# Kernel optimization log

Hardware: AMD Instinct MI355X
Metric: run time of the kernel (lower is better)

The kernel has to match this reference:

```python
import jax, jax.numpy as jnp
import numpy as np

INPUT_DIM = 64
HIDDEN_DIM = 32


def setup_inputs() -> dict:
    key = jax.random.key(0)
    ks = jax.random.split(key, 9)
    B, C, H, W = 8, INPUT_DIM, 64, 64
    s_in = 1.0 / np.sqrt(C)
    inp = {
        "h": jax.random.normal(ks[0], (B, C, H, W), dtype=jnp.float32),
        # 1x1 conv weights stored as [out, in]
        "wq": jax.random.uniform(ks[1], (HIDDEN_DIM, C), jnp.float32, -s_in, s_in),
        "bq": jax.random.uniform(ks[2], (HIDDEN_DIM,), jnp.float32, -s_in, s_in),
        "wk": jax.random.uniform(ks[3], (HIDDEN_DIM, C), jnp.float32, -s_in, s_in),
        "bk": jax.random.uniform(ks[4], (HIDDEN_DIM,), jnp.float32, -s_in, s_in),
        "wv": jax.random.uniform(ks[5], (C, C), jnp.float32, -s_in, s_in),
        "bv": jax.random.uniform(ks[6], (C,), jnp.float32, -s_in, s_in),
        "wz": jax.random.uniform(ks[7], (C, C), jnp.float32, -s_in, s_in),
        "bz": jax.random.uniform(ks[8], (C,), jnp.float32, -s_in, s_in),
    }
    return inp


def reference(h, wq, bq, wk, bk, wv, bv, wz, bz):
    B, C, H, W = h.shape
    N = H * W
    x = h.reshape(B, C, N)  # [B, C, N]
    # 1x1 convs == channel-wise linear maps
    q = jnp.einsum('oc,bcn->bno', wq, x) + bq          # [B, N, Dh]
    k = jnp.einsum('oc,bcn->bon', wk, x) + bk[:, None]  # [B, Dh, N]
    v = jnp.einsum('oc,bcn->bon', wv, x) + bv[:, None]  # [B, C, N]
    attn = jax.nn.softmax(jnp.einsum('bnd,bdm->bnm', q, k), axis=-1)  # [B, N, N]
    z = jnp.einsum('bnm,bcm->bcn', attn, v)             # [B, C, N]
    out = jnp.einsum('oc,bcn->bon', wz, z) + bz[:, None]
    return out.reshape(B, C, H, W) + h
```

## Files before the change

kernel.cpp:

```cpp
#include <hip/hip_runtime.h>
#include <stdint.h>

#define BATCH 8
#define CIN   64
#define DH    32
#define NTOK  4096
#define LOG2E 1.4426950408889634f

typedef float    f4   __attribute__((ext_vector_type(4)));
typedef short    s8v  __attribute__((ext_vector_type(8)));
typedef uint32_t u32;
typedef uint32_t u32x2 __attribute__((ext_vector_type(2)));
typedef uint32_t u32x4 __attribute__((ext_vector_type(4)));

static __device__ __forceinline__ short f2bf(float f) {
    union { float f; u32 u; } c; c.f = f;
    u32 u = c.u;
    u32 r = (u + 0x7fffu + ((u >> 16) & 1u)) >> 16;
    return (short)(r & 0xffffu);
}
static __device__ __forceinline__ u32 pk2(float a, float b) {
    return (u32)(uint16_t)f2bf(a) | ((u32)(uint16_t)f2bf(b) << 16);
}
static __device__ __forceinline__ u32 pktr(float a, float b) {
    union { float f; u32 u; } ca, cb; ca.f = a; cb.f = b;
#if __has_builtin(__builtin_amdgcn_perm)
    return __builtin_amdgcn_perm(cb.u, ca.u, 0x07060302u);
#else
    return (cb.u & 0xffff0000u) | (ca.u >> 16);
#endif
}
static __device__ __forceinline__ float bfhi(u32 u) {
    union { u32 u; float f; } c; c.u = u & 0xffff0000u; return c.f;
}
static __device__ __forceinline__ float bflo(u32 u) {
    union { u32 u; float f; } c; c.u = u << 16; return c.f;
}

__global__ __launch_bounds__(256) void proj_kernel(
    const float* __restrict__ h,
    const float* __restrict__ wq, const float* __restrict__ bq,
    const float* __restrict__ wk, const float* __restrict__ bk,
    const float* __restrict__ wv, const float* __restrict__ bv,
    short* __restrict__ qbf, short* __restrict__ kbf, short* __restrict__ vp)
{
    __shared__ short xT [64 * 72];
    __shared__ short wqs[32 * 72];
    __shared__ short wks[32 * 72];
    __shared__ short wvs[64 * 72];
    __shared__ short vls2[64 * 68];
    __shared__ float bqs[32], bks[32], bvs[64];

    const int t   = threadIdx.x;
    const int b   = blockIdx.x;
    const int nt0 = blockIdx.y * 64;

    {
        const int c  = t >> 2;
        const int ng = (t & 3) * 16;
        const float* src = h + ((size_t)(b * CIN + c)) * NTOK + nt0 + ng;
        f4 x0 = *(const f4*)(src + 0);
        f4 x1 = *(const f4*)(src + 4);
        f4 x2 = *(const f4*)(src + 8);
        f4 x3 = *(const f4*)(src + 12);
        #pragma unroll
        for (int i = 0; i < 4; ++i) {
            xT[(ng + 0  + i) * 72 + c] = f2bf(x0[i]);
            xT[(ng + 4  + i) * 72 + c] = f2bf(x1[i]);
            xT[(ng + 8  + i) * 72 + c] = f2bf(x2[i]);
            xT[(ng + 12 + i) * 72 + c] = f2bf(x3[i]);
        }
    }
    for (int idx = t; idx < 2048; idx += 256) {
        int o = idx >> 6, c = idx & 63;
        wqs[o * 72 + c] = f2bf(wq[idx] * LOG2E);
        wks[o * 72 + c] = f2bf(wk[idx]);
    }
    for (int idx = t; idx < 4096; idx += 256)
        wvs[(idx >> 6) * 72 + (idx & 63)] = f2bf(wv[idx]);
    if (t < 32) { bqs[t] = bq[t] * LOG2E; bks[t] = bk[t]; }
    if (t < 64) bvs[t] = bv[t];
    __syncthreads();

    const int w    = t >> 6;
    const int ln   = t & 15;
    const int quad = (t >> 4) & 3;
    const int nl   = w * 16 + ln;
    const int n    = nt0 + nl;
    const f4 zf4 = {0.f, 0.f, 0.f, 0.f};

    const s8v xb0 = *(const s8v*)&xT[nl * 72 + quad * 8];
    const s8v xb1 = *(const s8v*)&xT[nl * 72 + 32 + quad * 8];

    #pragma unroll
    for (int ot = 0; ot < 2; ++ot) {
        s8v a0 = *(const s8v*)&wqs[(ot * 16 + ln) * 72 + quad * 8];
        s8v a1 = *(const s8v*)&wqs[(ot * 16 + ln) * 72 + 32 + quad * 8];
        f4 d = __builtin_amdgcn_mfma_f32_16x16x32_bf16(a0, xb0, zf4, 0, 0, 0);
        d     = __builtin_amdgcn_mfma_f32_16x16x32_bf16(a1, xb1, d,  0, 0, 0);
        f4 bb = *(const f4*)&bqs[ot * 16 + quad * 4];
        u32x2 pw; pw[0] = pk2(d[0] + bb[0], d[1] + bb[1]);
                  pw[1] = pk2(d[2] + bb[2], d[3] + bb[3]);
        *(u32x2*)(qbf + ((size_t)(b * NTOK + n)) * DH + ot * 16 + quad * 4) = pw;

        s8v c0 = *(const s8v*)&wks[(ot * 16 + ln) * 72 + quad * 8];
        s8v c1 = *(const s8v*)&wks[(ot * 16 + ln) * 72 + 32 + quad * 8];
        f4 e = __builtin_amdgcn_mfma_f32_16x16x32_bf16(c0, xb0, zf4, 0, 0, 0);
        e     = __builtin_amdgcn_mfma_f32_16x16x32_bf16(c1, xb1, e,  0, 0, 0);
        f4 kb = *(const f4*)&bks[ot * 16 + quad * 4];
        u32x2 kw; kw[0] = pk2(e[0] + kb[0], e[1] + kb[1]);
                  kw[1] = pk2(e[2] + kb[2], e[3] + kb[3]);
        *(u32x2*)(kbf + ((size_t)(b * NTOK + n)) * DH + ot * 16 + quad * 4) = kw;
    }

    {
        const int p    = nl & 31;
        const int row  = (nl >> 5) * 32 + ((p >> 2) & 3) * 8
                       + (p >> 4) * 4 + (p & 3);
        short* vrow = &vls2[row * 68];
        #pragma unroll
        for (int ot = 0; ot < 4; ++ot) {
            s8v a0 = *(const s8v*)&wvs[(ot * 16 + ln) * 72 + quad * 8];
            s8v a1 = *(const s8v*)&wvs[(ot * 16 + ln) * 72 + 32 + quad * 8];
            f4 d = __builtin_amdgcn_mfma_f32_16x16x32_bf16(a0, xb0, zf4, 0, 0, 0);
            d     = __builtin_amdgcn_mfma_f32_16x16x32_bf16(a1, xb1, d,  0, 0, 0);
            const int ch = ot * 16 + quad * 4;
            u32x2 pw;
            pw[0] = pk2(d[0] + bvs[ch],     d[1] + bvs[ch + 1]);
            pw[1] = pk2(d[2] + bvs[ch + 2], d[3] + bvs[ch + 3]);
            *(u32x2*)&vrow[ch] = pw;
        }
    }
    __syncthreads();

    {
        const int g = t >> 5;
        const int r = t & 31;
        short tmp[16];
        #pragma unroll
        for (int j = 0; j < 8; ++j)
            #pragma unroll
            for (int cc = 0; cc < 2; ++cc)
                tmp[cc * 8 + j] = vls2[(g * 8 + j) * 68 + r * 2 + cc];
        u32x4* dst = (u32x4*)(vp + ((size_t)(b * 128 + blockIdx.y * 2) * 4) * 64 * 8);
        #pragma unroll
        for (int i = 0; i < 2; ++i)
            dst[t * 2 + i] = ((const u32x4*)tmp)[i];
    }
}

__global__ __launch_bounds__(256, 2) void attn_kernel(
    const float* __restrict__ h,  const float* __restrict__ wz,
    const float* __restrict__ bz,
    const short* __restrict__ qbf, const short* __restrict__ kbf,
    const short* __restrict__ vp,  float* __restrict__ out)
{
    __shared__ short accb[4][64][72];
    __shared__ short zbuf[64][72];
    __shared__ float lbuf[4][64];

    const int b    = blockIdx.x;
    const int qb0  = blockIdx.y * 64;
    const int tid  = threadIdx.x;
    const int w    = tid >> 6;
    const int lane = tid & 63;
    const int ln   = lane & 15;
    const int quad = lane >> 4;
    const f4 zf4 = {0.f, 0.f, 0.f, 0.f};

    s8v qf[4];
    #pragma unroll
    for (int f = 0; f < 4; ++f)
        qf[f] = *(const s8v*)(qbf + ((size_t)(b * NTOK + qb0 + f * 16 + ln)) * DH + quad * 8);

    f4 acc[4][4];
    f4 accl[4];
    #pragma unroll
    for (int f = 0; f < 4; ++f) {
        accl[f] = zf4;
        #pragma unroll
        for (int ct = 0; ct < 4; ++ct) acc[f][ct] = zf4;
    }
    s8v ones;
    #pragma unroll
    for (int j = 0; j < 8; ++j) ones[j] = (short)0x3F80;

    const short* kb2 = kbf + ((size_t)b * NTOK + w * 1024) * DH;
    const s8v*   vb2 = (const s8v*)(vp + (size_t)b * NTOK * CIN)
                     + (size_t)(w * 32) * 4 * 64;

    for (int kt = 0; kt < 1024; kt += 32) {
        const short* kp = kb2 + kt * DH;
        s8v kk0 = *(const s8v*)(kp + ln * DH + quad * 8);
        s8v kk1 = *(const s8v*)(kp + (16 + ln) * DH + quad * 8);
        const s8v* vg = vb2 + (size_t)((kt >> 5) * 4 + quad) * 64 + ln;
        s8v v0 = vg[0], v1 = vg[16], v2 = vg[32], v3 = vg[48];

        #pragma unroll
        for (int f = 0; f < 4; ++f) {
            f4 sa = __builtin_amdgcn_mfma_f32_16x16x32_bf16(kk0, qf[f], zf4, 0, 0, 0);
            f4 sb = __builtin_amdgcn_mfma_f32_16x16x32_bf16(kk1, qf[f], zf4, 0, 0, 0);
            f4 ea, eb;
            #pragma unroll
            for (int r = 0; r < 4; ++r) {
                ea[r] = __builtin_amdgcn_exp2f(sa[r]);
                eb[r] = __builtin_amdgcn_exp2f(sb[r]);
            }
            u32x4 pd;
            pd[0] = pktr(ea[0], ea[1]); pd[1] = pktr(ea[2], ea[3]);
            pd[2] = pktr(eb[0], eb[1]); pd[3] = pktr(eb[2], eb[3]);
            s8v pf = __builtin_bit_cast(s8v, pd);

            accl[f]   = __builtin_amdgcn_mfma_f32_16x16x32_bf16(ones, pf, accl[f],   0, 0, 0);
            acc[f][0] = __builtin_amdgcn_mfma_f32_16x16x32_bf16(v0,   pf, acc[f][0], 0, 0, 0);
            acc[f][1] = __builtin_amdgcn_mfma_f32_16x16x32_bf16(v1,   pf, acc[f][1], 0, 0, 0);
            acc[f][2] = __builtin_amdgcn_mfma_f32_16x16x32_bf16(v2,   pf, acc[f][2], 0, 0, 0);
            acc[f][3] = __builtin_amdgcn_mfma_f32_16x16x32_bf16(v3,   pf, acc[f][3], 0, 0, 0);
        }
    }

    if (quad == 0) {
        #pragma unroll
        for (int f = 0; f < 4; ++f) lbuf[w][f * 16 + ln] = accl[f][0];
    }
    #pragma unroll
    for (int f = 0; f < 4; ++f) {
        #pragma unroll
        for (int ct = 0; ct < 4; ++ct) {
            u32x2 pw;
            pw[0] = pk2(acc[f][ct][0], acc[f][ct][1]);
            pw[1] = pk2(acc[f][ct][2], acc[f][ct][3]);
            *(u32x2*)&accb[w][f * 16 + ln][ct * 16 + quad * 4] = pw;
        }
    }
    __syncthreads();

    {
        const int q   = tid >> 2;
        const int chg = (tid & 3) * 16;
        float ls = lbuf[0][q] + lbuf[1][q] + lbuf[2][q] + lbuf[3][q];
        float rl = __builtin_amdgcn_rcpf(ls);
        float zv[16];
        #pragma unroll
        for (int i = 0; i < 16; ++i) zv[i] = 0.f;
        #pragma unroll
        for (int w2 = 0; w2 < 4; ++w2) {
            u32x4 ua = *(u32x4*)&accb[w2][q][chg];
            u32x4 ub = *(u32x4*)&accb[w2][q][chg + 8];
            #pragma unroll
            for (int d = 0; d < 4; ++d) {
                zv[d * 2]     += bflo(ua[d]); zv[d * 2 + 1]     += bfhi(ua[d]);
                zv[8 + d * 2] += bflo(ub[d]); zv[8 + d * 2 + 1] += bfhi(ub[d]);
            }
        }
        u32x4 za, zb2;
        #pragma unroll
        for (int d = 0; d < 4; ++d) {
            za[d]  = pk2(zv[d * 2] * rl,     zv[d * 2 + 1] * rl);
            zb2[d] = pk2(zv[8 + d * 2] * rl, zv[8 + d * 2 + 1] * rl);
        }
        *(u32x4*)&zbuf[q][chg]     = za;
        *(u32x4*)&zbuf[q][chg + 8] = zb2;
    }
    __syncthreads();

    {
        const int ot = w;
        s8v wzf[2];
        #pragma unroll
        for (int half = 0; half < 2; ++half) {
            const float* wp = wz + (ot * 16 + ln) * 64 + half * 32 + quad * 8;
            f4 wa = *(const f4*)wp;
            f4 wb = *(const f4*)(wp + 4);
            u32x4 tt;
            tt[0] = pk2(wa[0], wa[1]); tt[1] = pk2(wa[2], wa[3]);
            tt[2] = pk2(wb[0], wb[1]); tt[3] = pk2(wb[2], wb[3]);
            wzf[half] = __builtin_bit_cast(s8v, tt);
        }
        f4 bzv = *(const f4*)(bz + ot * 16 + quad * 4);
        #pragma unroll
        for (int fi = 0; fi < 4; ++fi) {
            const int row = fi * 16 + ln;
            s8v z0 = *(const s8v*)&zbuf[row][quad * 8];
            s8v z1 = *(const s8v*)&zbuf[row][32 + quad * 8];
            f4 oa = __builtin_amdgcn_mfma_f32_16x16x32_bf16(wzf[0], z0, zf4, 0, 0, 0);
            oa     = __builtin_amdgcn_mfma_f32_16x16x32_bf16(wzf[1], z1, oa,  0, 0, 0);
            #pragma unroll
            for (int r = 0; r < 4; ++r) {
                size_t idx = ((size_t)(b * CIN + ot * 16 + quad * 4 + r)) * NTOK
                           + qb0 + row;
                out[idx] = oa[r] + bzv[r] + h[idx];
            }
        }
    }
}

extern "C" void kernel_launch(void* const* d_in, const int* in_sizes, int n_in,
                              void* d_out, int out_size, void* d_ws, size_t ws_size,
                              hipStream_t stream) {
    (void)in_sizes; (void)n_in; (void)out_size; (void)ws_size;
    const float* h  = (const float*)d_in[0];
    const float* wq = (const float*)d_in[1];
    const float* bq = (const float*)d_in[2];
    const float* wk = (const float*)d_in[3];
    const float* bk = (const float*)d_in[4];
    const float* wv = (const float*)d_in[5];
    const float* bv = (const float*)d_in[6];
    const float* wz = (const float*)d_in[7];
    const float* bz = (const float*)d_in[8];
    float* out = (float*)d_out;

    short* qbf = (short*)d_ws;
    short* kbf = qbf + (size_t)BATCH * NTOK * DH;
    short* vpw = kbf + (size_t)BATCH * NTOK * DH;

    proj_kernel<<<dim3(8, 64), dim3(256), 0, stream>>>(
        h, wq, bq, wk, bk, wv, bv, qbf, kbf, vpw);
    attn_kernel<<<dim3(8, 64), dim3(256), 0, stream>>>(
        h, wz, bz, qbf, kbf, vpw, out);
}
```

Measured before the change: 115.7 us.

## Share K/V tiles across two query groups via LDS staging in larger blocks

```diff
diff --git a/kernel.cpp b/kernel.cpp
--- a/kernel.cpp
+++ b/kernel.cpp
@@ -149,29 +149,37 @@
     }
 }
 
-__global__ __launch_bounds__(256, 2) void attn_kernel(
+__global__ __launch_bounds__(512, 2) void attn_kernel(
     const float* __restrict__ h,  const float* __restrict__ wz,
     const float* __restrict__ bz,
     const short* __restrict__ qbf, const short* __restrict__ kbf,
     const short* __restrict__ vp,  float* __restrict__ out)
 {
-    __shared__ short accb[4][64][72];
-    __shared__ short zbuf[64][72];
-    __shared__ float lbuf[4][64];
+    __shared__ short kst[4 * 3072];
+    __shared__ short accb[128 * 72];
+    __shared__ short zbuf[128 * 72];
+    __shared__ float lbuf[128];
 
     const int b    = blockIdx.x;
-    const int qb0  = blockIdx.y * 64;
+    const int qb0  = blockIdx.y * 128;
     const int tid  = threadIdx.x;
     const int w    = tid >> 6;
     const int lane = tid & 63;
     const int ln   = lane & 15;
     const int quad = lane >> 4;
+    const int qg   = w & 1;
+    const int kh   = w >> 1;
     const f4 zf4 = {0.f, 0.f, 0.f, 0.f};
 
+    short* stage = &kst[kh * 3072];
+    const short* kb = kbf + ((size_t)b * NTOK + kh * 1024) * DH;
+    const short* vb = vp  + (size_t)(b * 128 + kh * 32) * 4 * 64 * 8;
+
     s8v qf[4];
     #pragma unroll
     for (int f = 0; f < 4; ++f)
-        qf[f] = *(const s8v*)(qbf + ((size_t)(b * NTOK + qb0 + f * 16 + ln)) * DH + quad * 8);
+        qf[f] = *(const s8v*)(qbf +
+            ((size_t)(b * NTOK + qb0 + qg * 64 + f * 16 + ln)) * DH + quad * 8);
 
     f4 acc[4][4];
     f4 accl[4];
@@ -185,16 +193,41 @@
     #pragma unroll
     for (int j = 0; j < 8; ++j) ones[j] = (short)0x3F80;
 
-    const short* kb2 = kbf + ((size_t)b * NTOK + w * 1024) * DH;
-    const s8v*   vb2 = (const s8v*)(vp + (size_t)b * NTOK * CIN)
-                     + (size_t)(w * 32) * 4 * 64;
-
-    for (int kt = 0; kt < 1024; kt += 32) {
-        const short* kp = kb2 + kt * DH;
-        s8v kk0 = *(const s8v*)(kp + ln * DH + quad * 8);
-        s8v kk1 = *(const s8v*)(kp + (16 + ln) * DH + quad * 8);
-        const s8v* vg = vb2 + (size_t)((kt >> 5) * 4 + quad) * 64 + ln;
-        s8v v0 = vg[0], v1 = vg[16], v2 = vg[32], v3 = vg[48];
+    u32x4 r[3];
+    #pragma unroll
+    for (int j = 0; j < 3; ++j) {
+        const int c = qg * 3 + j;
+        const short* src = (c < 2) ? (kb + c * 512 + lane * 8)
+                                   : (vb + (c - 2) * 512 + lane * 8);
+        r[j] = *(const u32x4*)src;
+    }
+
+    for (int it = 0; it < 32; ++it) {
+        __syncthreads();
+        #pragma unroll
+        for (int j = 0; j < 3; ++j) {
+            const int c = qg * 3 + j;
+            *(u32x4*)&stage[c * 512 + lane * 8] = r[j];
+        }
+        __syncthreads();
+        if (it + 1 < 32) {
+            const short* ks = kb + (it + 1) * 1024;
+            const short* vs = vb + (it + 1) * 2048;
+            #pragma unroll
+            for (int j = 0; j < 3; ++j) {
+                const int c = qg * 3 + j;
+                const short* src = (c < 2) ? (ks + c * 512 + lane * 8)
+                                           : (vs + (c - 2) * 512 + lane * 8);
+                r[j] = *(const u32x4*)src;
+            }
+        }
+
+        s8v kk0 = *(const s8v*)&stage[ln * 32 + quad * 8];
+        s8v kk1 = *(const s8v*)&stage[(16 + ln) * 32 + quad * 8];
+        s8v v0 = *(const s8v*)&stage[1024 + (quad * 64 +  0 + ln) * 8];
+        s8v v1 = *(const s8v*)&stage[1024 + (quad * 64 + 16 + ln) * 8];
+        s8v v2 = *(const s8v*)&stage[1024 + (quad * 64 + 32 + ln) * 8];
+        s8v v3 = *(const s8v*)&stage[1024 + (quad * 64 + 48 + ln) * 8];
 
         #pragma unroll
         for (int f = 0; f < 4; ++f) {
@@ -202,9 +235,9 @@
             f4 sb = __builtin_amdgcn_mfma_f32_16x16x32_bf16(kk1, qf[f], zf4, 0, 0, 0);
             f4 ea, eb;
             #pragma unroll
-            for (int r = 0; r < 4; ++r) {
-                ea[r] = __builtin_amdgcn_exp2f(sa[r]);
-                eb[r] = __builtin_amdgcn_exp2f(sb[r]);
+            for (int rr = 0; rr < 4; ++rr) {
+                ea[rr] = __builtin_amdgcn_exp2f(sa[rr]);
+                eb[rr] = __builtin_amdgcn_exp2f(sb[rr]);
             }
             u32x4 pd;
             pd[0] = pktr(ea[0], ea[1]); pd[1] = pktr(ea[2], ea[3]);
@@ -219,53 +252,56 @@
         }
     }
 
-    if (quad == 0) {
-        #pragma unroll
-        for (int f = 0; f < 4; ++f) lbuf[w][f * 16 + ln] = accl[f][0];
-    }
-    #pragma unroll
-    for (int f = 0; f < 4; ++f) {
-        #pragma unroll
-        for (int ct = 0; ct < 4; ++ct) {
-            u32x2 pw;
-            pw[0] = pk2(acc[f][ct][0], acc[f][ct][1]);
-            pw[1] = pk2(acc[f][ct][2], acc[f][ct][3]);
-            *(u32x2*)&accb[w][f * 16 + ln][ct * 16 + quad * 4] = pw;
+    for (int ph = 1; ph < 4; ++ph) {
+        if (kh == ph) {
+            #pragma unroll
+            for (int f = 0; f < 4; ++f) {
+                const int row = qg * 64 + f * 16 + ln;
+                if (quad == 0) lbuf[row] = accl[f][0];
+                #pragma unroll
+                for (int ct = 0; ct < 4; ++ct) {
+                    u32x2 pw;
+                    pw[0] = pk2(acc[f][ct][0], acc[f][ct][1]);
+                    pw[1] = pk2(acc[f][ct][2], acc[f][ct][3]);
+                    *(u32x2*)&accb[row * 72 + ct * 16 + quad * 4] = pw;
+                }
+            }
+        }
+        __syncthreads();
+        if (kh == 0) {
+            #pragma unroll
+            for (int f = 0; f < 4; ++f) {
+                const int row = qg * 64 + f * 16 + ln;
+                accl[f][0] += lbuf[row];
+                #pragma unroll
+                for (int ct = 0; ct < 4; ++ct) {
+                    u32x2 pw = *(const u32x2*)&accb[row * 72 + ct * 16 + quad * 4];
+                    acc[f][ct][0] += bflo(pw[0]); acc[f][ct][1] += bfhi(pw[0]);
+                    acc[f][ct][2] += bflo(pw[1]); acc[f][ct][3] += bfhi(pw[1]);
+                }
+            }
+        }
+        __syncthreads();
+    }
+
+    if (kh == 0) {
+        #pragma unroll
+        for (int f = 0; f < 4; ++f) {
+            const float rl = __builtin_amdgcn_rcpf(accl[f][0]);
+            const int row = qg * 64 + f * 16 + ln;
+            #pragma unroll
+            for (int ct = 0; ct < 4; ++ct) {
+                u32x2 pw;
+                pw[0] = pk2(acc[f][ct][0] * rl, acc[f][ct][1] * rl);
+                pw[1] = pk2(acc[f][ct][2] * rl, acc[f][ct][3] * rl);
+                *(u32x2*)&zbuf[row * 72 + ct * 16 + quad * 4] = pw;
+            }
         }
     }
     __syncthreads();
 
     {
-        const int q   = tid >> 2;
-        const int chg = (tid & 3) * 16;
-        float ls = lbuf[0][q] + lbuf[1][q] + lbuf[2][q] + lbuf[3][q];
-        float rl = __builtin_amdgcn_rcpf(ls);
-        float zv[16];
-        #pragma unroll
-        for (int i = 0; i < 16; ++i) zv[i] = 0.f;
-        #pragma unroll
-        for (int w2 = 0; w2 < 4; ++w2) {
-            u32x4 ua = *(u32x4*)&accb[w2][q][chg];
-            u32x4 ub = *(u32x4*)&accb[w2][q][chg + 8];
-            #pragma unroll
-            for (int d = 0; d < 4; ++d) {
-                zv[d * 2]     += bflo(ua[d]); zv[d * 2 + 1]     += bfhi(ua[d]);
-                zv[8 + d * 2] += bflo(ub[d]); zv[8 + d * 2 + 1] += bfhi(ub[d]);
-            }
-        }
-        u32x4 za, zb2;
-        #pragma unroll
-        for (int d = 0; d < 4; ++d) {
-            za[d]  = pk2(zv[d * 2] * rl,     zv[d * 2 + 1] * rl);
-            zb2[d] = pk2(zv[8 + d * 2] * rl, zv[8 + d * 2 + 1] * rl);
-        }
-        *(u32x4*)&zbuf[q][chg]     = za;
-        *(u32x4*)&zbuf[q][chg + 8] = zb2;
-    }
-    __syncthreads();
-
-    {
-        const int ot = w;
+        const int ot = w & 3, qg2 = w >> 2;
         s8v wzf[2];
         #pragma unroll
         for (int half = 0; half < 2; ++half) {
@@ -280,16 +316,16 @@
         f4 bzv = *(const f4*)(bz + ot * 16 + quad * 4);
         #pragma unroll
         for (int fi = 0; fi < 4; ++fi) {
-            const int row = fi * 16 + ln;
-            s8v z0 = *(const s8v*)&zbuf[row][quad * 8];
-            s8v z1 = *(const s8v*)&zbuf[row][32 + quad * 8];
+            const int row = qg2 * 64 + fi * 16 + ln;
+            s8v z0 = *(const s8v*)&zbuf[row * 72 + quad * 8];
+            s8v z1 = *(const s8v*)&zbuf[row * 72 + 32 + quad * 8];
             f4 oa = __builtin_amdgcn_mfma_f32_16x16x32_bf16(wzf[0], z0, zf4, 0, 0, 0);
             oa     = __builtin_amdgcn_mfma_f32_16x16x32_bf16(wzf[1], z1, oa,  0, 0, 0);
             #pragma unroll
-            for (int r = 0; r < 4; ++r) {
-                size_t idx = ((size_t)(b * CIN + ot * 16 + quad * 4 + r)) * NTOK
+            for (int rr = 0; rr < 4; ++rr) {
+                size_t idx = ((size_t)(b * CIN + ot * 16 + quad * 4 + rr)) * NTOK
                            + qb0 + row;
-                out[idx] = oa[r] + bzv[r] + h[idx];
+                out[idx] = oa[rr] + bzv[rr] + h[idx];
             }
         }
     }
@@ -316,6 +352,6 @@
 
     proj_kernel<<<dim3(8, 64), dim3(256), 0, stream>>>(
         h, wq, bq, wk, bk, wv, bv, qbf, kbf, vpw);
-    attn_kernel<<<dim3(8, 64), dim3(256), 0, stream>>>(
+    attn_kernel<<<dim3(8, 32), dim3(512), 0, stream>>>(
         h, wz, bz, qbf, kbf, vpw, out);
 }
```

Result: slower. 122.9 us (+6.2%).

## Tree-reduce wave partials through two LDS slots, prefetch K/V, raise occupancy

Applied to the files above, without the earlier changes.

```diff
diff --git a/kernel.cpp b/kernel.cpp
--- a/kernel.cpp
+++ b/kernel.cpp
@@ -149,15 +149,15 @@
     }
 }
 
-__global__ __launch_bounds__(256, 2) void attn_kernel(
+__global__ __launch_bounds__(256, 3) void attn_kernel(
     const float* __restrict__ h,  const float* __restrict__ wz,
     const float* __restrict__ bz,
     const short* __restrict__ qbf, const short* __restrict__ kbf,
     const short* __restrict__ vp,  float* __restrict__ out)
 {
-    __shared__ short accb[4][64][72];
-    __shared__ short zbuf[64][72];
-    __shared__ float lbuf[4][64];
+    __shared__ short slotA[64 * 72];
+    __shared__ short slotB[64 * 72];
+    __shared__ float lbuf[2][64];
 
     const int b    = blockIdx.x;
     const int qb0  = blockIdx.y * 64;
@@ -189,12 +189,19 @@
     const s8v*   vb2 = (const s8v*)(vp + (size_t)b * NTOK * CIN)
                      + (size_t)(w * 32) * 4 * 64;
 
+    s8v kk0 = *(const s8v*)(kb2 + ln * DH + quad * 8);
+    s8v kk1 = *(const s8v*)(kb2 + (16 + ln) * DH + quad * 8);
+    const s8v* vg0 = vb2 + (size_t)quad * 64 + ln;
+    s8v v0 = vg0[0], v1 = vg0[16], v2 = vg0[32], v3 = vg0[48];
+
+    #pragma unroll 2
     for (int kt = 0; kt < 1024; kt += 32) {
-        const short* kp = kb2 + kt * DH;
-        s8v kk0 = *(const s8v*)(kp + ln * DH + quad * 8);
-        s8v kk1 = *(const s8v*)(kp + (16 + ln) * DH + quad * 8);
-        const s8v* vg = vb2 + (size_t)((kt >> 5) * 4 + quad) * 64 + ln;
-        s8v v0 = vg[0], v1 = vg[16], v2 = vg[32], v3 = vg[48];
+        const int ktn = (kt + 32) & 1023;
+        const short* kp = kb2 + ktn * DH;
+        s8v nk0 = *(const s8v*)(kp + ln * DH + quad * 8);
+        s8v nk1 = *(const s8v*)(kp + (16 + ln) * DH + quad * 8);
+        const s8v* vg = vb2 + (size_t)((ktn >> 5) * 4 + quad) * 64 + ln;
+        s8v nv0 = vg[0], nv1 = vg[16], nv2 = vg[32], nv3 = vg[48];
 
         #pragma unroll
         for (int f = 0; f < 4; ++f) {
@@ -217,50 +224,61 @@
             acc[f][2] = __builtin_amdgcn_mfma_f32_16x16x32_bf16(v2,   pf, acc[f][2], 0, 0, 0);
             acc[f][3] = __builtin_amdgcn_mfma_f32_16x16x32_bf16(v3,   pf, acc[f][3], 0, 0, 0);
         }
-    }
-
-    if (quad == 0) {
-        #pragma unroll
-        for (int f = 0; f < 4; ++f) lbuf[w][f * 16 + ln] = accl[f][0];
-    }
-    #pragma unroll
-    for (int f = 0; f < 4; ++f) {
-        #pragma unroll
-        for (int ct = 0; ct < 4; ++ct) {
-            u32x2 pw;
-            pw[0] = pk2(acc[f][ct][0], acc[f][ct][1]);
-            pw[1] = pk2(acc[f][ct][2], acc[f][ct][3]);
-            *(u32x2*)&accb[w][f * 16 + ln][ct * 16 + quad * 4] = pw;
-        }
-    }
-    __syncthreads();
-
-    {
-        const int q   = tid >> 2;
-        const int chg = (tid & 3) * 16;
-        float ls = lbuf[0][q] + lbuf[1][q] + lbuf[2][q] + lbuf[3][q];
-        float rl = __builtin_amdgcn_rcpf(ls);
-        float zv[16];
-        #pragma unroll
-        for (int i = 0; i < 16; ++i) zv[i] = 0.f;
-        #pragma unroll
-        for (int w2 = 0; w2 < 4; ++w2) {
-            u32x4 ua = *(u32x4*)&accb[w2][q][chg];
-            u32x4 ub = *(u32x4*)&accb[w2][q][chg + 8];
+        kk0 = nk0; kk1 = nk1;
+        v0 = nv0; v1 = nv1; v2 = nv2; v3 = nv3;
+    }
+
+    #define WRITE_SLOT(SLOT, LIDX)                                              \
+        {                                                                       \
+            _Pragma("unroll")                                                   \
+            for (int f = 0; f < 4; ++f) {                                       \
+                const int row = f * 16 + ln;                                    \
+                if (quad == 0) lbuf[LIDX][row] = accl[f][0];                    \
+                _Pragma("unroll")                                               \
+                for (int ct = 0; ct < 4; ++ct) {                                \
+                    u32x2 pw;                                                   \
+                    pw[0] = pk2(acc[f][ct][0], acc[f][ct][1]);                  \
+                    pw[1] = pk2(acc[f][ct][2], acc[f][ct][3]);                  \
+                    *(u32x2*)&SLOT[row * 72 + ct * 16 + quad * 4] = pw;         \
+                }                                                               \
+            }                                                                   \
+        }
+    #define ADD_SLOT(SLOT, LIDX)                                                \
+        {                                                                       \
+            _Pragma("unroll")                                                   \
+            for (int f = 0; f < 4; ++f) {                                       \
+                const int row = f * 16 + ln;                                    \
+                accl[f][0] += lbuf[LIDX][row];                                  \
+                _Pragma("unroll")                                               \
+                for (int ct = 0; ct < 4; ++ct) {                                \
+                    u32x2 pw = *(const u32x2*)&SLOT[row * 72 + ct * 16 + quad * 4]; \
+                    acc[f][ct][0] += bflo(pw[0]); acc[f][ct][1] += bfhi(pw[0]); \
+                    acc[f][ct][2] += bflo(pw[1]); acc[f][ct][3] += bfhi(pw[1]); \
+                }                                                               \
+            }                                                                   \
+        }
+    if (w == 1) WRITE_SLOT(slotA, 0);
+    if (w == 3) WRITE_SLOT(slotB, 1);
+    __syncthreads();
+    if (w == 0) ADD_SLOT(slotA, 0);
+    if (w == 2) ADD_SLOT(slotB, 1);
+    __syncthreads();
+    if (w == 2) WRITE_SLOT(slotA, 0);
+    __syncthreads();
+    if (w == 0) {
+        ADD_SLOT(slotA, 0);
+        #pragma unroll
+        for (int f = 0; f < 4; ++f) {
+            const float rl = __builtin_amdgcn_rcpf(accl[f][0]);
+            const int row = f * 16 + ln;
             #pragma unroll
-            for (int d = 0; d < 4; ++d) {
-                zv[d * 2]     += bflo(ua[d]); zv[d * 2 + 1]     += bfhi(ua[d]);
-                zv[8 + d * 2] += bflo(ub[d]); zv[8 + d * 2 + 1] += bfhi(ub[d]);
+            for (int ct = 0; ct < 4; ++ct) {
+                u32x2 pw;
+                pw[0] = pk2(acc[f][ct][0] * rl, acc[f][ct][1] * rl);
+                pw[1] = pk2(acc[f][ct][2] * rl, acc[f][ct][3] * rl);
+                *(u32x2*)&slotB[row * 72 + ct * 16 + quad * 4] = pw;
             }
         }
-        u32x4 za, zb2;
-        #pragma unroll
-        for (int d = 0; d < 4; ++d) {
-            za[d]  = pk2(zv[d * 2] * rl,     zv[d * 2 + 1] * rl);
-            zb2[d] = pk2(zv[8 + d * 2] * rl, zv[8 + d * 2 + 1] * rl);
-        }
-        *(u32x4*)&zbuf[q][chg]     = za;
-        *(u32x4*)&zbuf[q][chg + 8] = zb2;
     }
     __syncthreads();
 
@@ -281,8 +299,8 @@
         #pragma unroll
         for (int fi = 0; fi < 4; ++fi) {
             const int row = fi * 16 + ln;
-            s8v z0 = *(const s8v*)&zbuf[row][quad * 8];
-            s8v z1 = *(const s8v*)&zbuf[row][32 + quad * 8];
+            s8v z0 = *(const s8v*)&slotB[row * 72 + quad * 8];
+            s8v z1 = *(const s8v*)&slotB[row * 72 + 32 + quad * 8];
             f4 oa = __builtin_amdgcn_mfma_f32_16x16x32_bf16(wzf[0], z0, zf4, 0, 0, 0);
             oa     = __builtin_amdgcn_mfma_f32_16x16x32_bf16(wzf[1], z1, oa,  0, 0, 0);
             #pragma unroll
```

Result: slower. 123.0 us (+6.3%).

## Split attention key range across eight waves per block

Applied to the files above, without the earlier changes.

```diff
diff --git a/kernel.cpp b/kernel.cpp
--- a/kernel.cpp
+++ b/kernel.cpp
@@ -149,15 +149,15 @@
     }
 }
 
-__global__ __launch_bounds__(256, 2) void attn_kernel(
+__global__ __launch_bounds__(512, 4) void attn_kernel(
     const float* __restrict__ h,  const float* __restrict__ wz,
     const float* __restrict__ bz,
     const short* __restrict__ qbf, const short* __restrict__ kbf,
     const short* __restrict__ vp,  float* __restrict__ out)
 {
-    __shared__ short accb[4][64][72];
-    __shared__ short zbuf[64][72];
-    __shared__ float lbuf[4][64];
+    __shared__ short slots[8][64 * 68];
+    __shared__ float lbuf[8][64];
+    short* zbuf = (short*)slots;
 
     const int b    = blockIdx.x;
     const int qb0  = blockIdx.y * 64;
@@ -185,11 +185,11 @@
     #pragma unroll
     for (int j = 0; j < 8; ++j) ones[j] = (short)0x3F80;
 
-    const short* kb2 = kbf + ((size_t)b * NTOK + w * 1024) * DH;
+    const short* kb2 = kbf + ((size_t)b * NTOK + w * 512) * DH;
     const s8v*   vb2 = (const s8v*)(vp + (size_t)b * NTOK * CIN)
-                     + (size_t)(w * 32) * 4 * 64;
-
-    for (int kt = 0; kt < 1024; kt += 32) {
+                     + (size_t)(w * 16) * 4 * 64;
+
+    for (int kt = 0; kt < 512; kt += 32) {
         const short* kp = kb2 + kt * DH;
         s8v kk0 = *(const s8v*)(kp + ln * DH + quad * 8);
         s8v kk1 = *(const s8v*)(kp + (16 + ln) * DH + quad * 8);
@@ -219,70 +219,69 @@
         }
     }
 
-    if (quad == 0) {
-        #pragma unroll
-        for (int f = 0; f < 4; ++f) lbuf[w][f * 16 + ln] = accl[f][0];
-    }
     #pragma unroll
     for (int f = 0; f < 4; ++f) {
+        const int row = f * 16 + ln;
+        if (quad == 0) lbuf[w][row] = accl[f][0];
         #pragma unroll
         for (int ct = 0; ct < 4; ++ct) {
             u32x2 pw;
             pw[0] = pk2(acc[f][ct][0], acc[f][ct][1]);
             pw[1] = pk2(acc[f][ct][2], acc[f][ct][3]);
-            *(u32x2*)&accb[w][f * 16 + ln][ct * 16 + quad * 4] = pw;
+            *(u32x2*)&slots[w][row * 68 + ct * 16 + quad * 4] = pw;
         }
     }
     __syncthreads();
 
     {
-        const int q   = tid >> 2;
-        const int chg = (tid & 3) * 16;
-        float ls = lbuf[0][q] + lbuf[1][q] + lbuf[2][q] + lbuf[3][q];
-        float rl = __builtin_amdgcn_rcpf(ls);
-        float zv[16];
-        #pragma unroll
-        for (int i = 0; i < 16; ++i) zv[i] = 0.f;
-        #pragma unroll
-        for (int w2 = 0; w2 < 4; ++w2) {
-            u32x4 ua = *(u32x4*)&accb[w2][q][chg];
-            u32x4 ub = *(u32x4*)&accb[w2][q][chg + 8];
-            #pragma unroll
-            for (int d = 0; d < 4; ++d) {
-                zv[d * 2]     += bflo(ua[d]); zv[d * 2 + 1]     += bfhi(ua[d]);
-                zv[8 + d * 2] += bflo(ub[d]); zv[8 + d * 2 + 1] += bfhi(ub[d]);
-            }
-        }
-        u32x4 za, zb2;
-        #pragma unroll
-        for (int d = 0; d < 4; ++d) {
-            za[d]  = pk2(zv[d * 2] * rl,     zv[d * 2 + 1] * rl);
-            zb2[d] = pk2(zv[8 + d * 2] * rl, zv[8 + d * 2 + 1] * rl);
-        }
-        *(u32x4*)&zbuf[q][chg]     = za;
-        *(u32x4*)&zbuf[q][chg + 8] = zb2;
+        const int q = tid >> 3;
+        const int e = (tid & 7) * 8;
+        float ls = 0.f;
+        #pragma unroll
+        for (int s = 0; s < 8; ++s) ls += lbuf[s][q];
+        const float rl = __builtin_amdgcn_rcpf(ls);
+        float zv[8];
+        #pragma unroll
+        for (int i = 0; i < 8; ++i) zv[i] = 0.f;
+        #pragma unroll
+        for (int s = 0; s < 8; ++s) {
+            u32x2 a = *(const u32x2*)&slots[s][q * 68 + e];
+            u32x2 c = *(const u32x2*)&slots[s][q * 68 + e + 4];
+            zv[0] += bflo(a[0]); zv[1] += bfhi(a[0]);
+            zv[2] += bflo(a[1]); zv[3] += bfhi(a[1]);
+            zv[4] += bflo(c[0]); zv[5] += bfhi(c[0]);
+            zv[6] += bflo(c[1]); zv[7] += bfhi(c[1]);
+        }
+        __syncthreads();
+        u32x2 o0, o1;
+        o0[0] = pk2(zv[0] * rl, zv[1] * rl);
+        o0[1] = pk2(zv[2] * rl, zv[3] * rl);
+        o1[0] = pk2(zv[4] * rl, zv[5] * rl);
+        o1[1] = pk2(zv[6] * rl, zv[7] * rl);
+        *(u32x2*)&zbuf[q * 72 + e]     = o0;
+        *(u32x2*)&zbuf[q * 72 + e + 4] = o1;
     }
     __syncthreads();
 
     {
-        const int ot = w;
+        const int ot = w & 3, half = w >> 2;
         s8v wzf[2];
         #pragma unroll
-        for (int half = 0; half < 2; ++half) {
-            const float* wp = wz + (ot * 16 + ln) * 64 + half * 32 + quad * 8;
+        for (int hh = 0; hh < 2; ++hh) {
+            const float* wp = wz + (ot * 16 + ln) * 64 + hh * 32 + quad * 8;
             f4 wa = *(const f4*)wp;
             f4 wb = *(const f4*)(wp + 4);
             u32x4 tt;
             tt[0] = pk2(wa[0], wa[1]); tt[1] = pk2(wa[2], wa[3]);
             tt[2] = pk2(wb[0], wb[1]); tt[3] = pk2(wb[2], wb[3]);
-            wzf[half] = __builtin_bit_cast(s8v, tt);
+            wzf[hh] = __builtin_bit_cast(s8v, tt);
         }
         f4 bzv = *(const f4*)(bz + ot * 16 + quad * 4);
         #pragma unroll
-        for (int fi = 0; fi < 4; ++fi) {
-            const int row = fi * 16 + ln;
-            s8v z0 = *(const s8v*)&zbuf[row][quad * 8];
-            s8v z1 = *(const s8v*)&zbuf[row][32 + quad * 8];
+        for (int fi = 0; fi < 2; ++fi) {
+            const int row = (half * 2 + fi) * 16 + ln;
+            s8v z0 = *(const s8v*)&zbuf[row * 72 + quad * 8];
+            s8v z1 = *(const s8v*)&zbuf[row * 72 + 32 + quad * 8];
             f4 oa = __builtin_amdgcn_mfma_f32_16x16x32_bf16(wzf[0], z0, zf4, 0, 0, 0);
             oa     = __builtin_amdgcn_mfma_f32_16x16x32_bf16(wzf[1], z1, oa,  0, 0, 0);
             #pragma unroll
@@ -316,6 +315,6 @@
 
     proj_kernel<<<dim3(8, 64), dim3(256), 0, stream>>>(
         h, wq, bq, wk, bk, wv, bv, qbf, kbf, vpw);
-    attn_kernel<<<dim3(8, 64), dim3(256), 0, stream>>>(
+    attn_kernel<<<dim3(8, 64), dim3(512), 0, stream>>>(
         h, wz, bz, qbf, kbf, vpw, out);
 }
```

After: 210.6 us. 1.82x slower.
